# Kernel tuning notes

Measured on AMD Instinct MI355X. Metric: run time of the kernel, lower is better.

The kernel has to match this reference:

```python
import jax, jax.numpy as jnp
import numpy as np

N, F_IN, F_OUT, N_HEAD = 4096, 256, 64, 4
EDGE_P = 0.01  # sparsity of the random adjacency


def setup_inputs() -> dict:
    key = jax.random.key(0)
    k_h, k_adj, k_w, k_as, k_ad = jax.random.split(key, 5)
    h = jax.random.normal(k_h, (N, F_IN), dtype=jnp.float32)
    # random boolean adjacency with self-loops so every softmax row is valid
    adj = jax.random.uniform(k_adj, (N, N)) < EDGE_P
    adj = adj | jnp.eye(N, dtype=bool)
    # xavier_uniform-style params
    lim_w = float(np.sqrt(6.0 / (F_IN + F_OUT)))
    lim_a = float(np.sqrt(6.0 / (F_OUT + 1)))
    w = jax.random.uniform(k_w, (N_HEAD, F_IN, F_OUT), minval=-lim_w, maxval=lim_w, dtype=jnp.float32)
    a_src = jax.random.uniform(k_as, (N_HEAD, F_OUT, 1), minval=-lim_a, maxval=lim_a, dtype=jnp.float32)
    a_dst = jax.random.uniform(k_ad, (N_HEAD, F_OUT, 1), minval=-lim_a, maxval=lim_a, dtype=jnp.float32)
    bias = jnp.zeros((F_OUT,), dtype=jnp.float32)
    return {"h": h, "adj": adj, "w": w, "a_src": a_src, "a_dst": a_dst, "bias": bias}


def reference(h, adj, w, a_src, a_dst, bias):
    # h_prime[k] = h @ w[k]  -> [H, n, f_out]
    h_prime = jnp.einsum('nf,hfo->hno', h, w)
    # attention logits: attn[k,i,j] = src[k,i] + dst[k,j]
    src = jnp.einsum('hno,ho->hn', h_prime, a_src[..., 0])  # [H, n]
    dst = jnp.einsum('hno,ho->hn', h_prime, a_dst[..., 0])  # [H, n]
    scores = src[:, :, None] + dst[:, None, :]              # [H, n, n]
    scores = jnp.where(scores >= 0, scores, 0.2 * scores)   # leaky_relu(0.2)
    neg = jnp.asarray(jnp.finfo(scores.dtype).min, scores.dtype)
    scores = jnp.where(adj[None, :, :], scores, neg)
    attn = jax.nn.softmax(scores, axis=-1)                  # [H, n, n]
    out = jnp.einsum('hij,hjo->iho', attn, h_prime)         # [n, H, f_out]
    return out + bias
```

## Files before the change

kernel.cpp:

```cpp
#include <hip/hip_runtime.h>

#define NN 4096
#define FIN 256
#define FOUT 64
#define NH 4
#define CAP 128
#define HPAD 264

typedef __attribute__((ext_vector_type(8))) short bf16x8;
typedef __attribute__((ext_vector_type(4))) float f32x4;

__device__ __forceinline__ unsigned short f2bf(float f) {
    unsigned u = __float_as_uint(f);
    u = (u + 0x7fff + ((u >> 16) & 1)) >> 16;
    return (unsigned short)u;
}

__global__ __launch_bounds__(256) void gat_mfma(
    const float* __restrict__ h, const float* __restrict__ w,
    const float* __restrict__ a_src, const float* __restrict__ a_dst,
    float* __restrict__ h_prime, float* __restrict__ src, float* __restrict__ dst)
{
    const int b = blockIdx.x, t = threadIdx.x;
    const int head = b & 3, n0 = (b >> 2) * 64;
    const int wv = t >> 6, lane = t & 63;
    const int lrow = lane & 15, lk8 = lane >> 4;

    __shared__ unsigned short hs[64 * HPAD];
    __shared__ unsigned short ws[64 * HPAD];

#pragma unroll
    for (int i = 0; i < 16; ++i) {
        const int idx = t + i * 256;
        const int row = idx >> 6, f4 = idx & 63;
        const float4 v = *(const float4*)(h + (size_t)(n0 + row) * FIN + f4 * 4);
        ushort4 o;
        o.x = f2bf(v.x); o.y = f2bf(v.y); o.z = f2bf(v.z); o.w = f2bf(v.w);
        *(ushort4*)&hs[row * HPAD + f4 * 4] = o;
    }
    {
        const int kb = t >> 4, o4 = t & 15;
#pragma unroll
        for (int i = 0; i < 16; ++i) {
            const int k = kb + i * 16;
            const float4 v = *(const float4*)(w + ((size_t)head * FIN + k) * FOUT + o4 * 4);
            ws[(o4 * 4 + 0) * HPAD + k] = f2bf(v.x);
            ws[(o4 * 4 + 1) * HPAD + k] = f2bf(v.y);
            ws[(o4 * 4 + 2) * HPAD + k] = f2bf(v.z);
            ws[(o4 * 4 + 3) * HPAD + k] = f2bf(v.w);
        }
    }
    __syncthreads();

    bf16x8 a[8];
#pragma unroll
    for (int ks = 0; ks < 8; ++ks)
        a[ks] = *(const bf16x8*)&hs[(wv * 16 + lrow) * HPAD + ks * 32 + lk8 * 8];

    f32x4 acc[4] = {{0.f,0.f,0.f,0.f},{0.f,0.f,0.f,0.f},
                    {0.f,0.f,0.f,0.f},{0.f,0.f,0.f,0.f}};
#pragma unroll
    for (int ks = 0; ks < 8; ++ks) {
#pragma unroll
        for (int nt = 0; nt < 4; ++nt) {
            const bf16x8 bf = *(const bf16x8*)&ws[(nt * 16 + lrow) * HPAD + ks * 32 + lk8 * 8];
            acc[nt] = __builtin_amdgcn_mfma_f32_16x16x32_bf16(a[ks], bf, acc[nt], 0, 0, 0);
        }
    }

    const int mbase = n0 + wv * 16 + lk8 * 4;
#pragma unroll
    for (int nt = 0; nt < 4; ++nt)
#pragma unroll
        for (int r = 0; r < 4; ++r)
            h_prime[((size_t)head * NN + mbase + r) * FOUT + nt * 16 + lrow] = acc[nt][r];

    float as_nt[4], ad_nt[4];
#pragma unroll
    for (int nt = 0; nt < 4; ++nt) {
        as_nt[nt] = a_src[head * FOUT + nt * 16 + lrow];
        ad_nt[nt] = a_dst[head * FOUT + nt * 16 + lrow];
    }
    float psr[4] = {0.f,0.f,0.f,0.f}, pdr[4] = {0.f,0.f,0.f,0.f};
#pragma unroll
    for (int nt = 0; nt < 4; ++nt)
#pragma unroll
        for (int r = 0; r < 4; ++r) {
            psr[r] = fmaf(acc[nt][r], as_nt[nt], psr[r]);
            pdr[r] = fmaf(acc[nt][r], ad_nt[nt], pdr[r]);
        }
#pragma unroll
    for (int r = 0; r < 4; ++r)
#pragma unroll
        for (int off = 1; off <= 8; off <<= 1) {
            psr[r] += __shfl_xor(psr[r], off, 64);
            pdr[r] += __shfl_xor(pdr[r], off, 64);
        }
    if (lrow == 0)
#pragma unroll
        for (int r = 0; r < 4; ++r) {
            src[head * NN + mbase + r] = psr[r];
            dst[head * NN + mbase + r] = pdr[r];
        }
}

__global__ __launch_bounds__(256) void gat_scanbits(
    const int* __restrict__ adj, unsigned long long* __restrict__ bits)
{
    const int lane = threadIdx.x & 63;
    const int nvec = NN * NN / 4;
    const int step = 2048 * 256;
    for (int g = blockIdx.x * 256 + threadIdx.x; g < nvec; g += step) {
        const int4 a = ((const int4*)adj)[g];
        const unsigned long long b0 = __ballot(a.x != 0);
        const unsigned long long b1 = __ballot(a.y != 0);
        const unsigned long long b2 = __ballot(a.z != 0);
        const unsigned long long b3 = __ballot(a.w != 0);
        const int row = g >> 10;
        const int it  = (g >> 6) & 15;
        unsigned long long mk = b0;
        mk = ((lane & 3) == 1) ? b1 : mk;
        mk = ((lane & 3) == 2) ? b2 : mk;
        mk = ((lane & 3) == 3) ? b3 : mk;
        if (lane < 4) bits[(size_t)row * 64 + it * 4 + lane] = mk;
    }
}

__global__ __launch_bounds__(256) void gat_attn(
    const unsigned long long* __restrict__ bits,
    const float* __restrict__ h_prime, const float* __restrict__ src,
    const float* __restrict__ dst, const float* __restrict__ bias,
    float* __restrict__ out)
{
    const int i = blockIdx.x, t = threadIdx.x, wv = t >> 6, lane = t & 63;

    __shared__ int   idx_l[CAP];
    __shared__ float sc[NH][CAP];
    __shared__ int   cnt;
    __shared__ float inv_sum[NH];

    if (wv == 0) {
        unsigned long long m = bits[(size_t)i * 64 + lane];
        const int c = __popcll(m);
        int pre = c;
#pragma unroll
        for (int off = 1; off < 64; off <<= 1) {
            const int nb = __shfl_up(pre, off, 64);
            if (lane >= off) pre += nb;
        }
        int p = pre - c;
        const int cb = (lane >> 2) * 256 + (lane & 3);
        while (m) {
            const int bpos = __ffsll((unsigned long long)m) - 1;
            if (p < CAP) idx_l[p] = cb + 4 * bpos;
            ++p;
            m &= m - 1;
        }
        if (lane == 63) cnt = pre;
    }
    __syncthreads();

    const int count = min(cnt, CAP);
    const int cpad  = (count + 7) & ~7;

    if (t < count) {
        const int j = idx_l[t];
#pragma unroll
        for (int hh = 0; hh < NH; ++hh) {
            const float v = src[hh * NN + i] + dst[hh * NN + j];
            sc[hh][t] = (v >= 0.f) ? v : 0.2f * v;
        }
    } else if (t < cpad) {
        idx_l[t] = 0;
#pragma unroll
        for (int hh = 0; hh < NH; ++hh) sc[hh][t] = 0.f;
    }
    __syncthreads();

    {
        float m = -3.4e38f;
        for (int p = lane; p < count; p += 64) m = fmaxf(m, sc[wv][p]);
#pragma unroll
        for (int off = 32; off >= 1; off >>= 1) m = fmaxf(m, __shfl_xor(m, off, 64));
        float e = 0.f;
        for (int p = lane; p < count; p += 64) {
            const float v = __expf(sc[wv][p] - m);
            sc[wv][p] = v;
            e += v;
        }
#pragma unroll
        for (int off = 32; off >= 1; off >>= 1) e += __shfl_xor(e, off, 64);
        if (lane == 0) inv_sum[wv] = 1.f / e;
    }
    __syncthreads();

    float accv = 0.f;
    const float* hp = h_prime + (size_t)(wv * NN) * FOUT + lane;
    for (int p0 = 0; p0 < cpad; p0 += 8) {
        int jj[8]; float vv[8]; float ww[8];
#pragma unroll
        for (int k = 0; k < 8; ++k) jj[k] = idx_l[p0 + k];
#pragma unroll
        for (int k = 0; k < 8; ++k) vv[k] = hp[(size_t)jj[k] * FOUT];
#pragma unroll
        for (int k = 0; k < 8; ++k) ww[k] = sc[wv][p0 + k];
#pragma unroll
        for (int k = 0; k < 8; ++k) accv = fmaf(ww[k], vv[k], accv);
    }
    out[(size_t)i * (NH * FOUT) + wv * FOUT + lane] = accv * inv_sum[wv] + bias[lane];
}

extern "C" void kernel_launch(void* const* d_in, const int* in_sizes, int n_in,
                              void* d_out, int out_size, void* d_ws, size_t ws_size,
                              hipStream_t stream) {
    const float* h     = (const float*)d_in[0];
    const int*   adj   = (const int*)d_in[1];
    const float* w     = (const float*)d_in[2];
    const float* a_src = (const float*)d_in[3];
    const float* a_dst = (const float*)d_in[4];
    const float* bias  = (const float*)d_in[5];
    float* out = (float*)d_out;

    float* wsf     = (float*)d_ws;
    float* h_prime = wsf;
    float* src     = h_prime + NH * NN * FOUT;
    float* dst     = src + NH * NN;
    unsigned long long* bits = (unsigned long long*)(dst + NH * NN);

    gat_mfma<<<256, 256, 0, stream>>>(h, w, a_src, a_dst, h_prime, src, dst);
    gat_scanbits<<<2048, 256, 0, stream>>>(adj, bits);
    gat_attn<<<NN, 256, 0, stream>>>(bits, h_prime, src, dst, bias, out);
}
```

Before: 42.28 us.

## Fuse projection GEMM and adjacency bit-packing into one heterogeneous launch

Merges the MFMA projection kernel and the adjacency scan kernel into a single launch. The first 256 blocks do the GEMM and the remaining 1024 blocks each pack four adjacency rows, so the two independent phases run concurrently and one launch is saved. The W operand is now staged in LDS directly in MFMA fragment order (bf16x8 per lane) instead of a transposed padded tile. The scan side now issues 16 int4 loads per lane up front. The combined block uses more LDS (hs plus a 32KB fragment buffer) even for the scan blocks, which can lower occupancy for the bandwidth-bound adjacency pass.

Result: faster. 37.31 us (-11.8%).

```diff
diff --git a/kernel.cpp b/kernel.cpp
--- a/kernel.cpp
+++ b/kernel.cpp
@@ -6,6 +6,8 @@
 #define NH 4
 #define CAP 128
 #define HPAD 264
+#define MFB 256
+#define CPB 1024
 
 typedef __attribute__((ext_vector_type(8))) short bf16x8;
 typedef __attribute__((ext_vector_type(4))) float f32x4;
@@ -16,113 +18,115 @@
     return (unsigned short)u;
 }
 
-__global__ __launch_bounds__(256) void gat_mfma(
-    const float* __restrict__ h, const float* __restrict__ w,
-    const float* __restrict__ a_src, const float* __restrict__ a_dst,
-    float* __restrict__ h_prime, float* __restrict__ src, float* __restrict__ dst)
+__global__ __launch_bounds__(256) void gat_prep(
+    const float* __restrict__ h, const int* __restrict__ adj,
+    const float* __restrict__ w, const float* __restrict__ a_src,
+    const float* __restrict__ a_dst,
+    float* __restrict__ h_prime, float* __restrict__ src, float* __restrict__ dst,
+    unsigned long long* __restrict__ bits)
 {
     const int b = blockIdx.x, t = threadIdx.x;
-    const int head = b & 3, n0 = (b >> 2) * 64;
     const int wv = t >> 6, lane = t & 63;
-    const int lrow = lane & 15, lk8 = lane >> 4;
-
-    __shared__ unsigned short hs[64 * HPAD];
-    __shared__ unsigned short ws[64 * HPAD];
-
-#pragma unroll
-    for (int i = 0; i < 16; ++i) {
-        const int idx = t + i * 256;
-        const int row = idx >> 6, f4 = idx & 63;
-        const float4 v = *(const float4*)(h + (size_t)(n0 + row) * FIN + f4 * 4);
-        ushort4 o;
-        o.x = f2bf(v.x); o.y = f2bf(v.y); o.z = f2bf(v.z); o.w = f2bf(v.w);
-        *(ushort4*)&hs[row * HPAD + f4 * 4] = o;
-    }
-    {
-        const int kb = t >> 4, o4 = t & 15;
+
+    __shared__ __align__(16) unsigned short hs[64 * HPAD];
+    __shared__ bf16x8 bfrag[2048];
+
+    if (b < MFB) {
+        const int head = b & 3, n0 = (b >> 2) * 64;
+        const int lrow = lane & 15, lk8 = lane >> 4;
+
 #pragma unroll
         for (int i = 0; i < 16; ++i) {
-            const int k = kb + i * 16;
-            const float4 v = *(const float4*)(w + ((size_t)head * FIN + k) * FOUT + o4 * 4);
-            ws[(o4 * 4 + 0) * HPAD + k] = f2bf(v.x);
-            ws[(o4 * 4 + 1) * HPAD + k] = f2bf(v.y);
-            ws[(o4 * 4 + 2) * HPAD + k] = f2bf(v.z);
-            ws[(o4 * 4 + 3) * HPAD + k] = f2bf(v.w);
-        }
-    }
-    __syncthreads();
-
-    bf16x8 a[8];
-#pragma unroll
-    for (int ks = 0; ks < 8; ++ks)
-        a[ks] = *(const bf16x8*)&hs[(wv * 16 + lrow) * HPAD + ks * 32 + lk8 * 8];
-
-    f32x4 acc[4] = {{0.f,0.f,0.f,0.f},{0.f,0.f,0.f,0.f},
-                    {0.f,0.f,0.f,0.f},{0.f,0.f,0.f,0.f}};
-#pragma unroll
-    for (int ks = 0; ks < 8; ++ks) {
+            const int idx = t + i * 256;
+            const int row = idx >> 6, f4 = idx & 63;
+            const float4 v = *(const float4*)(h + (size_t)(n0 + row) * FIN + f4 * 4);
+            ushort4 o;
+            o.x = f2bf(v.x); o.y = f2bf(v.y); o.z = f2bf(v.z); o.w = f2bf(v.w);
+            *(ushort4*)&hs[row * HPAD + f4 * 4] = o;
+        }
+#pragma unroll
+        for (int i = 0; i < 8; ++i) {
+            const int g = t + i * 256;
+            const int lg = g & 63, ks = (g >> 6) & 7, nt = g >> 9;
+            const int col = nt * 16 + (lg & 15);
+            const int kbase = ks * 32 + (lg >> 4) * 8;
+            const float* wp = w + ((size_t)head * FIN + kbase) * FOUT + col;
+            union { bf16x8 v; unsigned short s[8]; } u;
+#pragma unroll
+            for (int j = 0; j < 8; ++j) u.s[j] = f2bf(wp[j * FOUT]);
+            bfrag[g] = u.v;
+        }
+        __syncthreads();
+
+        bf16x8 a[8];
+#pragma unroll
+        for (int ks = 0; ks < 8; ++ks)
+            a[ks] = *(const bf16x8*)&hs[(wv * 16 + lrow) * HPAD + ks * 32 + lk8 * 8];
+
+        f32x4 acc[4] = {{0.f,0.f,0.f,0.f},{0.f,0.f,0.f,0.f},
+                        {0.f,0.f,0.f,0.f},{0.f,0.f,0.f,0.f}};
+#pragma unroll
+        for (int ks = 0; ks < 8; ++ks) {
+#pragma unroll
+            for (int nt = 0; nt < 4; ++nt)
+                acc[nt] = __builtin_amdgcn_mfma_f32_16x16x32_bf16(
+                              a[ks], bfrag[(nt * 8 + ks) * 64 + lane], acc[nt], 0, 0, 0);
+        }
+
+        const int mbase = n0 + wv * 16 + lk8 * 4;
+#pragma unroll
+        for (int nt = 0; nt < 4; ++nt)
+#pragma unroll
+            for (int r = 0; r < 4; ++r)
+                h_prime[((size_t)head * NN + mbase + r) * FOUT + nt * 16 + lrow] = acc[nt][r];
+
+        float as_nt[4], ad_nt[4];
 #pragma unroll
         for (int nt = 0; nt < 4; ++nt) {
-            const bf16x8 bf = *(const bf16x8*)&ws[(nt * 16 + lrow) * HPAD + ks * 32 + lk8 * 8];
-            acc[nt] = __builtin_amdgcn_mfma_f32_16x16x32_bf16(a[ks], bf, acc[nt], 0, 0, 0);
-        }
-    }
-
-    const int mbase = n0 + wv * 16 + lk8 * 4;
-#pragma unroll
-    for (int nt = 0; nt < 4; ++nt)
+            as_nt[nt] = a_src[head * FOUT + nt * 16 + lrow];
+            ad_nt[nt] = a_dst[head * FOUT + nt * 16 + lrow];
+        }
+        float psr[4] = {0.f,0.f,0.f,0.f}, pdr[4] = {0.f,0.f,0.f,0.f};
+#pragma unroll
+        for (int nt = 0; nt < 4; ++nt)
+#pragma unroll
+            for (int r = 0; r < 4; ++r) {
+                psr[r] = fmaf(acc[nt][r], as_nt[nt], psr[r]);
+                pdr[r] = fmaf(acc[nt][r], ad_nt[nt], pdr[r]);
+            }
 #pragma unroll
         for (int r = 0; r < 4; ++r)
-            h_prime[((size_t)head * NN + mbase + r) * FOUT + nt * 16 + lrow] = acc[nt][r];
-
-    float as_nt[4], ad_nt[4];
-#pragma unroll
-    for (int nt = 0; nt < 4; ++nt) {
-        as_nt[nt] = a_src[head * FOUT + nt * 16 + lrow];
-        ad_nt[nt] = a_dst[head * FOUT + nt * 16 + lrow];
-    }
-    float psr[4] = {0.f,0.f,0.f,0.f}, pdr[4] = {0.f,0.f,0.f,0.f};
-#pragma unroll
-    for (int nt = 0; nt < 4; ++nt)
-#pragma unroll
-        for (int r = 0; r < 4; ++r) {
-            psr[r] = fmaf(acc[nt][r], as_nt[nt], psr[r]);
-            pdr[r] = fmaf(acc[nt][r], ad_nt[nt], pdr[r]);
-        }
-#pragma unroll
-    for (int r = 0; r < 4; ++r)
-#pragma unroll
-        for (int off = 1; off <= 8; off <<= 1) {
-            psr[r] += __shfl_xor(psr[r], off, 64);
-            pdr[r] += __shfl_xor(pdr[r], off, 64);
-        }
-    if (lrow == 0)
-#pragma unroll
-        for (int r = 0; r < 4; ++r) {
-            src[head * NN + mbase + r] = psr[r];
-            dst[head * NN + mbase + r] = pdr[r];
-        }
-}
-
-__global__ __launch_bounds__(256) void gat_scanbits(
-    const int* __restrict__ adj, unsigned long long* __restrict__ bits)
-{
-    const int lane = threadIdx.x & 63;
-    const int nvec = NN * NN / 4;
-    const int step = 2048 * 256;
-    for (int g = blockIdx.x * 256 + threadIdx.x; g < nvec; g += step) {
-        const int4 a = ((const int4*)adj)[g];
-        const unsigned long long b0 = __ballot(a.x != 0);
-        const unsigned long long b1 = __ballot(a.y != 0);
-        const unsigned long long b2 = __ballot(a.z != 0);
-        const unsigned long long b3 = __ballot(a.w != 0);
-        const int row = g >> 10;
-        const int it  = (g >> 6) & 15;
-        unsigned long long mk = b0;
-        mk = ((lane & 3) == 1) ? b1 : mk;
-        mk = ((lane & 3) == 2) ? b2 : mk;
-        mk = ((lane & 3) == 3) ? b3 : mk;
-        if (lane < 4) bits[(size_t)row * 64 + it * 4 + lane] = mk;
+#pragma unroll
+            for (int off = 1; off <= 8; off <<= 1) {
+                psr[r] += __shfl_xor(psr[r], off, 64);
+                pdr[r] += __shfl_xor(pdr[r], off, 64);
+            }
+        if (lrow == 0)
+#pragma unroll
+            for (int r = 0; r < 4; ++r) {
+                src[head * NN + mbase + r] = psr[r];
+                dst[head * NN + mbase + r] = pdr[r];
+            }
+    } else {
+        const int row = (b - MFB) * 4 + wv;
+        const int4* arow = (const int4*)(adj + (size_t)row * NN);
+        int4 buf[16];
+#pragma unroll
+        for (int it = 0; it < 16; ++it) buf[it] = arow[it * 64 + lane];
+
+        unsigned long long* brow = bits + (size_t)row * 64;
+#pragma unroll
+        for (int it = 0; it < 16; ++it) {
+            const unsigned long long b0 = __ballot(buf[it].x != 0);
+            const unsigned long long b1 = __ballot(buf[it].y != 0);
+            const unsigned long long b2 = __ballot(buf[it].z != 0);
+            const unsigned long long b3 = __ballot(buf[it].w != 0);
+            unsigned long long mk = b0;
+            mk = ((lane & 3) == 1) ? b1 : mk;
+            mk = ((lane & 3) == 2) ? b2 : mk;
+            mk = ((lane & 3) == 3) ? b3 : mk;
+            if (lane < 4) brow[it * 4 + lane] = mk;
+        }
     }
 }
 
@@ -227,7 +231,7 @@
     float* dst     = src + NH * NN;
     unsigned long long* bits = (unsigned long long*)(dst + NH * NN);
 
-    gat_mfma<<<256, 256, 0, stream>>>(h, w, a_src, a_dst, h_prime, src, dst);
-    gat_scanbits<<<2048, 256, 0, stream>>>(adj, bits);
+    gat_prep<<<MFB + CPB, 256, 0, stream>>>(h, adj, w, a_src, a_dst,
+                                            h_prime, src, dst, bits);
     gat_attn<<<NN, 256, 0, stream>>>(bits, h_prime, src, dst, bias, out);
 }
```
